# Performance work log

Measured on AMD Instinct MI355X. Metric: run time of the kernel, lower is better.

Reference implementation:

```python
import jax, jax.numpy as jnp
import numpy as np

B, S, DIN, DIM = 4, 4096, 256, 256
GAMMA = 0.9865


def setup_inputs() -> dict:
    key = jax.random.key(0)
    ks = jax.random.split(key, 9)
    inp = {
        'xq': jax.random.normal(ks[0], (B, S, DIN), dtype=jnp.float32),
        'xk': jax.random.normal(ks[1], (B, S, DIN), dtype=jnp.float32),
        'xv': jax.random.normal(ks[2], (B, S, DIN), dtype=jnp.float32),
        'Wq': jax.random.normal(ks[3], (DIN, DIM), dtype=jnp.float32) * 0.05,
        'bq': jnp.zeros((DIM,), dtype=jnp.float32),
        'Wk': jax.random.normal(ks[4], (DIN, DIM), dtype=jnp.float32) * 0.05,
        'bk': jnp.zeros((DIM,), dtype=jnp.float32),
        'Wv': jax.random.normal(ks[5], (DIN, DIM), dtype=jnp.float32) * 0.05,
        'bv': jnp.zeros((DIM,), dtype=jnp.float32),
    }
    return inp


def _decay_matrix(s, gamma):
    # D[i, j] = gamma^(i-j) if i >= j else 0
    idx = jnp.arange(s)
    diff = idx[:, None] - idx[None, :]
    D = jnp.where(diff >= 0,
                  jnp.power(jnp.float32(gamma), diff.astype(jnp.float32)),
                  jnp.float32(0.0))
    return D


def reference(xq, xk, xv, Wq, bq, Wk, bk, Wv, bv):
    Q = xq @ Wq + bq  # [B,S,D]
    K = xk @ Wk + bk  # [B,S,D]
    V = xv @ Wv + bv  # [B,S,D]
    d = Q.shape[-1]
    # scores[b,i,j] = Q[b,i] . K[b,j] / sqrt(d)
    x = jnp.einsum('bid,bjd->bij', Q, K) / jnp.sqrt(jnp.float32(d))
    D = _decay_matrix(S, GAMMA)
    # Faithful to TF broadcasting: divides along the LAST axis (per-column by
    # sqrt of that index's row-sum): D[i,j] /= sqrt(sum_k D[j,k])
    D = D / jnp.sqrt(jnp.sum(D, axis=-1))
    x = x * D  # broadcast [B,S,S] * [S,S]
    # _norm_3 per batch element with TF broadcasting: x[b,i,j] /= max(|sum_k x[b,j,k]|, 1)
    denom = jnp.maximum(jnp.abs(jnp.sum(x, axis=-1)), 1.0)  # [B,S]
    x = x / denom[:, None, :]
    return x @ V  # [B,S,D]
```

## Files before the change

### kernel.cpp

```cpp
#include <hip/hip_runtime.h>
#include <math.h>

#define BB 4
#define SS 4096
#define DD 256
#define LL 256
#define NCH 16
#define GAMMA 0.9865f
#define LOG2G (-0.019609034f)
#define INV1MG 74.07407407f
#define SLAB 1032
#define SLABB 520

typedef __attribute__((ext_vector_type(8))) short short8;
typedef __attribute__((ext_vector_type(4))) float f32x4;
typedef unsigned short u16;
typedef unsigned int u32;

__device__ __forceinline__ u16 f2bf(float f) {
  union { float f; unsigned u; } v; v.f = f;
  unsigned r = v.u + 0x7FFFu + ((v.u >> 16) & 1u);
  return (u16)(r >> 16);
}
__device__ __forceinline__ float bf2f(u16 h) {
  union { unsigned u; float f; } v; v.u = ((unsigned)h) << 16; return v.f;
}

__device__ __forceinline__ void gll16(const u16* g, u16* l) {
  __builtin_amdgcn_global_load_lds(
      (const __attribute__((address_space(1))) u32*)g,
      (__attribute__((address_space(3))) u32*)l, 16, 0, 0);
}
__device__ __forceinline__ void stage8kp(const u16* g, u16* l, int lane) {
#pragma unroll
  for (int i = 0; i < 8; ++i)
    gll16(g + i * 512 + lane * 8, l + (i >> 1) * SLAB + (i & 1) * 512);
}
__device__ __forceinline__ void stageB64(const u16* g, u16* l, int lane) {
#pragma unroll
  for (int i = 0; i < 4; ++i)
    gll16(g + i * 1024 + lane * 8, l + i * SLABB);
}
__device__ __forceinline__ void stageAB(
    const u16* AhP, const u16* AlP, const u16* BhP, const u16* BlP, int ks,
    u16* Ab, u16* Bb, int wave, int lane)
{
  if (wave == 0) stage8kp(AhP + ks * 4096, Ab, lane);
  if (wave == 1) stage8kp(AlP + ks * 4096, Ab + 4 * SLAB, lane);
  if (wave == 2) stageB64(BhP + ks * 4096, Bb, lane);
  if (wave == 3) stageB64(BlP + ks * 4096, Bb + 4 * SLABB, lane);
}

__device__ __forceinline__ void mfma_step_slab(
    const u16* Ah, const u16* Al, const u16* Bh, const u16* Bl,
    int wm0, int wn0, int fm, int fq, f32x4 acc[4][4])
{
  const int ka = fq * SLAB;
  short8 ah[4], al[4];
#pragma unroll
  for (int i = 0; i < 4; ++i) {
    ah[i] = *(const short8*)&Ah[ka + (wm0 + i * 16 + fm) * 8];
    al[i] = *(const short8*)&Al[ka + (wm0 + i * 16 + fm) * 8];
  }
#pragma unroll
  for (int j = 0; j < 4; ++j) {
    short8 bh = *(const short8*)&Bh[ka + (wn0 + j * 16 + fm) * 8];
    short8 bl = *(const short8*)&Bl[ka + (wn0 + j * 16 + fm) * 8];
#pragma unroll
    for (int i = 0; i < 4; ++i) {
      acc[i][j] = __builtin_amdgcn_mfma_f32_16x16x32_bf16(al[i], bh, acc[i][j], 0, 0, 0);
      acc[i][j] = __builtin_amdgcn_mfma_f32_16x16x32_bf16(ah[i], bl, acc[i][j], 0, 0, 0);
      acc[i][j] = __builtin_amdgcn_mfma_f32_16x16x32_bf16(ah[i], bh, acc[i][j], 0, 0, 0);
    }
  }
}

__device__ __forceinline__ void mfma_step_ab(
    const u16* Ah, const u16* Al, const u16* Bh, const u16* Bl,
    int wm0, int wn0, int fm, int fq, f32x4 acc[4][2])
{
  const int ka = fq * SLAB, kb = fq * SLABB;
  short8 ah[4], al[4];
#pragma unroll
  for (int i = 0; i < 4; ++i) {
    ah[i] = *(const short8*)&Ah[ka + (wm0 + i * 16 + fm) * 8];
    al[i] = *(const short8*)&Al[ka + (wm0 + i * 16 + fm) * 8];
  }
#pragma unroll
  for (int j = 0; j < 2; ++j) {
    short8 bh = *(const short8*)&Bh[kb + (wn0 + j * 16 + fm) * 8];
    short8 bl = *(const short8*)&Bl[kb + (wn0 + j * 16 + fm) * 8];
#pragma unroll
    for (int i = 0; i < 4; ++i) {
      acc[i][j] = __builtin_amdgcn_mfma_f32_16x16x32_bf16(al[i], bh, acc[i][j], 0, 0, 0);
      acc[i][j] = __builtin_amdgcn_mfma_f32_16x16x32_bf16(ah[i], bl, acc[i][j], 0, 0, 0);
      acc[i][j] = __builtin_amdgcn_mfma_f32_16x16x32_bf16(ah[i], bh, acc[i][j], 0, 0, 0);
    }
  }
}

__device__ __forceinline__ void bounce_write(
    float* fb, const f32x4 acc[4][4], int wm0, int wn0, int fm, int fq, int p)
{
  if (wn0 == p * 64) {
#pragma unroll
    for (int i = 0; i < 4; ++i)
#pragma unroll
      for (int j = 0; j < 4; ++j)
#pragma unroll
        for (int r = 0; r < 4; ++r)
          fb[(wm0 + i * 16 + fq * 4 + r) * 65 + j * 16 + fm] = acc[i][j][r];
  }
}

__global__ __launch_bounds__(256) void init_pack_kernel(
    const float* __restrict__ Wq, const float* __restrict__ Wk, const float* __restrict__ Wv,
    u16* __restrict__ Wth, u16* __restrict__ Wtl,
    float* __restrict__ rsP, float* __restrict__ lVec)
{
  const int which = blockIdx.x;
  const int it = blockIdx.y;
  const int t = threadIdx.x;
  if (which == 0) {
    *(float4*)&rsP[(size_t)(it * 256 + t) * 4] = (float4){0.f, 0.f, 0.f, 0.f};
  } else if (which == 1) {
    *(float4*)&lVec[(size_t)(it * 256 + t) * 4] = (float4){0.f, 0.f, 0.f, 0.f};
  }
  const float* W = which == 0 ? Wq : (which == 1 ? Wk : Wv);
  for (int pn = 0; pn < 2; ++pn) {
    int pos = it * 256 + t;
    int k8 = pos >> 7, r = pos & 127;
    u16 hs[8], ls[8];
#pragma unroll
    for (int u = 0; u < 8; ++u) {
      float x = W[(size_t)(k8 * 8 + u) * DD + pn * 128 + r];
      u16 h = f2bf(x); hs[u] = h; ls[u] = f2bf(x - bf2f(h));
    }
    size_t o = ((size_t)((which * 2 + pn) * 32 + k8)) * 1024 + (size_t)r * 8;
    *(short8*)&Wth[o] = *(short8*)hs;
    *(short8*)&Wtl[o] = *(short8*)ls;
  }
}

__device__ __forceinline__ void loadX(float xs[2][8], const float* XP, int ks,
                                      int arow, int ak8) {
#pragma unroll
  for (int t = 0; t < 2; ++t) {
    const float* src = XP + (size_t)(t * 64 + arow) * DD + ks * 32 + ak8 * 8;
    *(float4*)&xs[t][0] = *(const float4*)src;
    *(float4*)&xs[t][4] = *(const float4*)(src + 4);
  }
}
__device__ __forceinline__ void writeAsplit(u16* Ab, const float xs[2][8],
                                            int arow, int ak8) {
#pragma unroll
  for (int t = 0; t < 2; ++t) {
    int row = t * 64 + arow;
    u16 hs[8], ls[8];
#pragma unroll
    for (int u = 0; u < 8; ++u) {
      u16 h = f2bf(xs[t][u]); hs[u] = h; ls[u] = f2bf(xs[t][u] - bf2f(h));
    }
    *(short8*)&Ab[ak8 * SLAB + row * 8] = *(short8*)hs;
    *(short8*)&Ab[4 * SLAB + ak8 * SLAB + row * 8] = *(short8*)ls;
  }
}

__global__ __launch_bounds__(256, 2) void proj_kernel(
    const float* __restrict__ xq, const float* __restrict__ xk, const float* __restrict__ xv,
    const u16* __restrict__ Wth, const u16* __restrict__ Wtl,
    const float* __restrict__ bq, const float* __restrict__ bk_, const float* __restrict__ bv,
    u16* __restrict__ Qh, u16* __restrict__ Ql,
    u16* __restrict__ Kh, u16* __restrict__ Kl,
    u16* __restrict__ KTh, u16* __restrict__ KTl, float* __restrict__ VT32,
    float* __restrict__ lVec)
{
  const int which = blockIdx.z;
  const float* bias = which == 0 ? bq : (which == 1 ? bk_ : bv);
  const int m0 = blockIdx.x * 128;
  const int pn = blockIdx.y;
  __shared__ u16 SM[2 * 16 * SLAB];
  __shared__ float rsc[128];
  __shared__ float wlut[128];
  __shared__ float kacc[64];
  float* fb = (float*)SM;
  const int tid = threadIdx.x, lane = tid & 63, wave = tid >> 6;
  const int wm0 = (wave >> 1) * 64, wn0 = (wave & 1) * 64;
  const int fm = lane & 15, fq = lane >> 4;
  if (which == 1) {
    if (tid < 128) {
      int sb = (m0 & (SS - 1)) + tid;
      rsc[tid] = rsqrtf((1.0f - exp2f((float)(sb + 1) * LOG2G)) * INV1MG);
      wlut[tid] = exp2f((float)(255 - ((m0 & (LL - 1)) + tid)) * LOG2G);
    }
    if (tid < 64) kacc[tid] = 0.f;
  }
  const float* XP = (which == 0 ? xq : (which == 1 ? xk : xv)) + (size_t)m0 * DD;
  const u16* WhP = Wth + (size_t)((which * 2 + pn) * 32) * 1024;
  const u16* WlP = Wtl + (size_t)((which * 2 + pn) * 32) * 1024;
  const int arow = tid >> 2, ak8 = tid & 3;
  f32x4 acc[4][4];
#pragma unroll
  for (int i = 0; i < 4; ++i)
#pragma unroll
    for (int j = 0; j < 4; ++j) acc[i][j] = (f32x4){0.f, 0.f, 0.f, 0.f};
  float xs[2][8];
  loadX(xs, XP, 0, arow, ak8);
  writeAsplit(SM, xs, arow, ak8);
  if (wave == 2) stage8kp(WhP, SM + 8 * SLAB, lane);
  if (wave == 3) stage8kp(WlP, SM + 12 * SLAB, lane);
  int cur = 0;
  for (int ks = 0; ks < 8; ++ks) {
    __syncthreads();
    u16* Bc = cur ? SM + 16 * SLAB : SM;
    u16* Bn = cur ? SM : SM + 16 * SLAB;
    if (ks < 7) {
      loadX(xs, XP, ks + 1, arow, ak8);
      if (wave == 2) stage8kp(WhP + (ks + 1) * 4096, Bn + 8 * SLAB, lane);
      if (wave == 3) stage8kp(WlP + (ks + 1) * 4096, Bn + 12 * SLAB, lane);
    }
    mfma_step_slab(Bc, Bc + 4 * SLAB, Bc + 8 * SLAB, Bc + 12 * SLAB,
                   wm0, wn0, fm, fq, acc);
    if (ks < 7) writeAsplit(Bn, xs, arow, ak8);
    cur ^= 1;
  }
  const int b = m0 >> 12, sbb = m0 & (SS - 1);
  for (int p = 0; p < 2; ++p) {
    __syncthreads();
    bounce_write(fb, acc, wm0, wn0, fm, fq, p);
    __syncthreads();
    if (which == 0) {
#pragma unroll
      for (int it = 0; it < 4; ++it) {
        int unit = it * 256 + tid;
        int k8l = unit >> 7, row = unit & 127;
        int gcol0 = pn * 128 + p * 64 + k8l * 8;
        u16 hs[8], ls[8];
#pragma unroll
        for (int u = 0; u < 8; ++u) {
          float v = (fb[row * 65 + k8l * 8 + u] + bias[gcol0 + u]) * (1.f / 16.f);
          u16 h = f2bf(v); hs[u] = h; ls[u] = f2bf(v - bf2f(h));
        }
        size_t o = (size_t)(m0 >> 7) * 32768 + (size_t)(pn * 16 + p * 8 + k8l) * 1024 + row * 8;
        *(short8*)&Qh[o] = *(short8*)hs;
        *(short8*)&Ql[o] = *(short8*)ls;
      }
    } else if (which == 1) {
#pragma unroll
      for (int it = 0; it < 4; ++it) {
        int unit = it * 256 + tid;
        int k8l = unit >> 7, row = unit & 127;
        int gcol0 = pn * 128 + p * 64 + k8l * 8;
        u16 hs[8], ls[8];
#pragma unroll
        for (int u = 0; u < 8; ++u) {
          float v = (fb[row * 65 + k8l * 8 + u] + bias[gcol0 + u]) * rsc[row];
          u16 h = f2bf(v); hs[u] = h; ls[u] = f2bf(v - bf2f(h));
        }
        size_t o = (size_t)(m0 >> 7) * 32768 + (size_t)(pn * 16 + p * 8 + k8l) * 1024 + row * 8;
        *(short8*)&Kh[o] = *(short8*)hs;
        *(short8*)&Kl[o] = *(short8*)ls;
      }
      float kpart = 0.f;
#pragma unroll
      for (int it = 0; it < 4; ++it) {
        int unit = it * 256 + tid;
        int dl = unit & 63, s8l = unit >> 6;
        int gcolg = pn * 128 + p * 64 + dl;
        float bs = bias[gcolg];
        u16 hs[8], ls[8];
#pragma unroll
        for (int u = 0; u < 8; ++u) {
          int row = s8l * 8 + u;
          float v = (fb[row * 65 + dl] + bs) * rsc[row];
          kpart = fmaf(v, wlut[row], kpart);
          u16 h = f2bf(v); hs[u] = h; ls[u] = f2bf(v - bf2f(h));
        }
        int sb0 = sbb + s8l * 8;
        size_t o = ((size_t)(b * 2 + (gcolg >> 7)) * 512 + (sb0 >> 3)) * 1024 + (size_t)(gcolg & 127) * 8;
        *(short8*)&KTh[o] = *(short8*)hs;
        *(short8*)&KTl[o] = *(short8*)ls;
      }
      atomicAdd(&kacc[tid & 63], kpart);
      __syncthreads();
      if (tid < 64) {
        int c = sbb >> 8;
        atomicAdd(&lVec[(size_t)(b * NCH + c) * DD + pn * 128 + p * 64 + tid], kacc[tid]);
        kacc[tid] = 0.f;
      }
    } else {
#pragma unroll
      for (int it = 0; it < 4; ++it) {
        int unit = it * 256 + tid;
        int dl = unit & 63, s8l = unit >> 6;
        int gcolg = pn * 128 + p * 64 + dl;
        float bs = bias[gcolg];
        float vv[8];
#pragma unroll
        for (int u = 0; u < 8; ++u) vv[u] = fb[(s8l * 8 + u) * 65 + dl] + bs;
        float* dst = &VT32[(size_t)b * DD * SS + (size_t)gcolg * SS + sbb + s8l * 8];
        *(float4*)dst = (float4){vv[0], vv[1], vv[2], vv[3]};
        *(float4*)(dst + 4) = (float4){vv[4], vv[5], vv[6], vv[7]};
      }
    }
  }
}

__global__ __launch_bounds__(256, 3) void scores_kernel(
    const u16* __restrict__ Qh, const u16* __restrict__ Ql,
    const u16* __restrict__ Kh, const u16* __restrict__ Kl,
    const float* __restrict__ lVec, u16* __restrict__ Sgh, u16* __restrict__ Sgl,
    float* __restrict__ rsP)
{
  const int chunk = blockIdx.x, b = chunk >> 4, c = chunk & 15;
  const int y = blockIdx.y;
  const int m0 = (y < 2) ? 0 : 128;
  const int jn0 = (y < 2) ? y * 64 : (y - 2) * 64;
  __shared__ u16 SA[2 * 8 * SLAB];
  __shared__ u16 SB[2 * 8 * SLABB];
  __shared__ float cv[256], lut[256], rowAcc[128], qd2[2][128];
  float* fb = (float*)SA;
  const int tid = threadIdx.x, lane = tid & 63, wave = tid >> 6;
  const int wm0 = (wave >> 1) * 64, wn0 = (wave & 1) * 32;
  const int fm = lane & 15, fq = lane >> 4;
  if (jn0 == 0) {
    const float gL = exp2f((float)LL * LOG2G);
    float s = 0.f;
    for (int cp = 0; cp < c; ++cp)
      s = fmaf(gL, s, lVec[(size_t)(b * NCH + cp) * DD + tid]);
    cv[tid] = s;
  }
  lut[tid] = exp2f((float)tid * LOG2G);
  if (tid < 128) rowAcc[tid] = 0.f;
  const int growA = b * SS + c * LL + m0;
  const int growB = b * SS + c * LL + jn0;
  const u16* QhP = Qh + (size_t)(growA >> 7) * 32768;
  const u16* QlP = Ql + (size_t)(growA >> 7) * 32768;
  const u16* KhP = Kh + (size_t)(growB >> 7) * 32768 + (size_t)(growB & 127) * 8;
  const u16* KlP = Kl + (size_t)(growB >> 7) * 32768 + (size_t)(growB & 127) * 8;
  f32x4 acc[4][2];
#pragma unroll
  for (int i = 0; i < 4; ++i)
#pragma unroll
    for (int j = 0; j < 2; ++j) acc[i][j] = (f32x4){0.f, 0.f, 0.f, 0.f};
  float qdreg = 0.f;
  const int qrow = tid & 127, qk8b = tid >> 7;
  stageAB(QhP, QlP, KhP, KlP, 0, SA, SB, wave, lane);
  int cur = 0;
  for (int ks = 0; ks < 8; ++ks) {
    __syncthreads();
    u16* Ac = cur ? SA + 8 * SLAB : SA;
    u16* Bc = cur ? SB + 8 * SLABB : SB;
    u16* An = cur ? SA : SA + 8 * SLAB;
    u16* Bn = cur ? SB : SB + 8 * SLABB;
    if (ks < 7) stageAB(QhP, QlP, KhP, KlP, ks + 1, An, Bn, wave, lane);
    mfma_step_ab(Ac, Ac + 4 * SLAB, Bc, Bc + 4 * SLABB, wm0, wn0, fm, fq, acc);
    if (jn0 == 0) {
#pragma unroll
      for (int h2 = 0; h2 < 2; ++h2) {
        int k8l = qk8b + 2 * h2;
        const u16* ahp = &Ac[k8l * SLAB + qrow * 8];
        const u16* alp = &Ac[4 * SLAB + k8l * SLAB + qrow * 8];
#pragma unroll
        for (int u = 0; u < 8; ++u)
          qdreg = fmaf(bf2f(ahp[u]) + bf2f(alp[u]), cv[ks * 32 + k8l * 8 + u], qdreg);
      }
    }
    cur ^= 1;
  }
  qd2[qk8b][qrow] = qdreg;
  const int ps = chunk * 2 + (m0 >> 7);
  for (int rh = 0; rh < 2; ++rh) {
    __syncthreads();
    if (wm0 == rh * 64) {
#pragma unroll
      for (int i = 0; i < 4; ++i)
#pragma unroll
        for (int j = 0; j < 2; ++j)
#pragma unroll
          for (int r = 0; r < 4; ++r)
            fb[(i * 16 + fq * 4 + r) * 65 + wn0 + j * 16 + fm] = acc[i][j][r];
    }
    __syncthreads();
#pragma unroll
    for (int it = 0; it < 2; ++it) {
      int unit = it * 256 + tid;
      int k8l = unit >> 6, rowl = unit & 63;
      int il = m0 + rh * 64 + rowl;
      int jlb = jn0 + k8l * 8;
      float part = 0.f;
      u16 hs[8], ls[8];
#pragma unroll
      for (int u = 0; u < 8; ++u) {
        int jl = jlb + u;
        float v = (jl <= il) ? fb[rowl * 65 + k8l * 8 + u] * lut[il - jl] : 0.f;
        part += v;
        u16 h = f2bf(v); hs[u] = h; ls[u] = f2bf(v - bf2f(h));
      }
      atomicAdd(&rowAcc[rh * 64 + rowl], part);
      size_t o = (size_t)(ps * 32 + (jn0 >> 3) + k8l) * 1024 + (size_t)(rh * 64 + rowl) * 8;
      *(short8*)&Sgh[o] = *(short8*)hs;
      *(short8*)&Sgl[o] = *(short8*)ls;
    }
  }
  __syncthreads();
  if (tid < 128) {
    float rs = rowAcc[tid];
    if (jn0 == 0)
      rs += exp2f((float)(m0 + tid + 1) * LOG2G) * (qd2[0][tid] + qd2[1][tid]);
    atomicAdd(&rsP[(size_t)b * SS + c * LL + m0 + tid], rs);
  }
}

__global__ __launch_bounds__(256) void vscale_kernel(
    const float* __restrict__ VT32, const float* __restrict__ rsP,
    u16* __restrict__ VdTh, u16* __restrict__ VdTl,
    u16* __restrict__ VwTh, u16* __restrict__ VwTl)
{
  const int x = blockIdx.x;
  const int b = x >> 6, pd = (x >> 5) & 1, sg = x & 31;
  const int t = threadIdx.x;
  __shared__ float tile[64][132];
  __shared__ float sdn[128], wtl[128];
  if (t < 128) {
    int s = sg * 128 + t;
    sdn[t] = fmaxf(fabsf(rsP[(size_t)b * SS + s]), 1.0f);
    wtl[t] = exp2f((float)(255 - (s & 255)) * LOG2G);
  }
  for (int eh = 0; eh < 2; ++eh) {
    __syncthreads();
#pragma unroll
    for (int v = 0; v < 8; ++v) {
      int lin = v * 256 + t;
      int col4 = lin & 31, row = lin >> 5;
      float4 xv = *(const float4*)&VT32[(size_t)b * DD * SS +
          (size_t)(pd * 128 + eh * 64 + row) * SS + sg * 128 + col4 * 4];
      *(float4*)&tile[row][col4 * 4] = xv;
    }
    __syncthreads();
#pragma unroll
    for (int it = 0; it < 4; ++it) {
      int unit = it * 256 + t;
      int s8l = unit >> 6, el = unit & 63;
      int e = pd * 128 + eh * 64 + el;
      u16 dh[8], dl_[8], wh[8], wl[8];
#pragma unroll
      for (int u = 0; u < 8; ++u) {
        int sloc = s8l * 8 + u;
        float vd = tile[el][sloc] / sdn[sloc];
        float vw = vd * wtl[sloc];
        u16 h = f2bf(vd); dh[u] = h; dl_[u] = f2bf(vd - bf2f(h));
        u16 h2 = f2bf(vw); wh[u] = h2; wl[u] = f2bf(vw - bf2f(h2));
      }
      int s8g = sg * 16 + s8l;
      size_t o = ((size_t)((b * 2 + pd) * 512 + s8g)) * 1024 + (size_t)(e & 127) * 8;
      *(short8*)&VdTh[o] = *(short8*)dh; *(short8*)&VdTl[o] = *(short8*)dl_;
      *(short8*)&VwTh[o] = *(short8*)wh; *(short8*)&VwTl[o] = *(short8*)wl;
    }
  }
}

__global__ __launch_bounds__(256, 3) void lmat_kernel(
    const u16* __restrict__ VwTh, const u16* __restrict__ VwTl,
    const u16* __restrict__ KTh, const u16* __restrict__ KTl,
    float* __restrict__ lMatT)
{
  const int chunk = blockIdx.x, b = chunk >> 4, c = chunk & 15;
  const int ty = blockIdx.y;
  const int m0 = (ty >> 2) * 128, n0 = (ty & 3) * 64;
  __shared__ u16 SA[2 * 8 * SLAB];
  __shared__ u16 SB[2 * 8 * SLABB];
  const int tid = threadIdx.x, lane = tid & 63, wave = tid >> 6;
  const int wm0 = (wave >> 1) * 64, wn0 = (wave & 1) * 32;
  const int fm = lane & 15, fq = lane >> 4;
  const u16* AhP = VwTh + ((size_t)(b * 2 + (m0 >> 7)) * 512 + c * 32) * 1024;
  const u16* AlP = VwTl + ((size_t)(b * 2 + (m0 >> 7)) * 512 + c * 32) * 1024;
  const u16* BhP = KTh + ((size_t)(b * 2 + (n0 >> 7)) * 512 + c * 32) * 1024 + (size_t)(n0 & 127) * 8;
  const u16* BlP = KTl + ((size_t)(b * 2 + (n0 >> 7)) * 512 + c * 32) * 1024 + (size_t)(n0 & 127) * 8;
  f32x4 acc[4][2];
#pragma unroll
  for (int i = 0; i < 4; ++i)
#pragma unroll
    for (int j = 0; j < 2; ++j) acc[i][j] = (f32x4){0.f, 0.f, 0.f, 0.f};
  stageAB(AhP, AlP, BhP, BlP, 0, SA, SB, wave, lane);
  int cur = 0;
  for (int ks = 0; ks < 8; ++ks) {
    __syncthreads();
    u16* Ac = cur ? SA + 8 * SLAB : SA;
    u16* Bc = cur ? SB + 8 * SLABB : SB;
    u16* An = cur ? SA : SA + 8 * SLAB;
    u16* Bn = cur ? SB : SB + 8 * SLABB;
    if (ks < 7) stageAB(AhP, AlP, BhP, BlP, ks + 1, An, Bn, wave, lane);
    mfma_step_ab(Ac, Ac + 4 * SLAB, Bc, Bc + 4 * SLABB, wm0, wn0, fm, fq, acc);
    cur ^= 1;
  }
#pragma unroll
  for (int i = 0; i < 4; ++i)
#pragma unroll
    for (int j = 0; j < 2; ++j)
#pragma unroll
      for (int r = 0; r < 4; ++r) {
        int e = m0 + wm0 + i * 16 + fq * 4 + r;
        int d = n0 + wn0 + j * 16 + fm;
        lMatT[(size_t)chunk * 65536 + (size_t)e * 256 + d] = acc[i][j][r];
      }
}

__global__ __launch_bounds__(256) void combine_mat_kernel(
    const float* __restrict__ lMatT, u16* __restrict__ cMh, u16* __restrict__ cMl)
{
  const int t = blockIdx.x * 256 + threadIdx.x;
  const int b = t >> 13, rem = t & 8191;
  const int k8 = rem >> 8, e = rem & 255;
  const float gL = powf(GAMMA, (float)LL);
  float s[8] = {0.f, 0.f, 0.f, 0.f, 0.f, 0.f, 0.f, 0.f};
  for (int ch = 0; ch < 16; ++ch) {
    size_t ro = (size_t)(b * 16 + ch) * 65536 + (size_t)e * 256 + k8 * 8;
    float4 a0 = *(const float4*)&lMatT[ro];
    float4 a1 = *(const float4*)&lMatT[ro + 4];
    float vals[8] = {a0.x, a0.y, a0.z, a0.w, a1.x, a1.y, a1.z, a1.w};
    u16 hh[8], ll[8];
#pragma unroll
    for (int u = 0; u < 8; ++u) {
      u16 h = f2bf(s[u]); hh[u] = h; ll[u] = f2bf(s[u] - bf2f(h));
    }
    size_t wo = ((size_t)(((b * 16 + ch) * 2 + (e >> 7)) * 32 + k8)) * 1024 + (size_t)(e & 127) * 8;
    *(short8*)&cMh[wo] = *(short8*)hh;
    *(short8*)&cMl[wo] = *(short8*)ll;
#pragma unroll
    for (int u = 0; u < 8; ++u) s[u] = gL * s[u] + vals[u];
  }
}

__global__ __launch_bounds__(256, 3) void out_kernel(
    const u16* __restrict__ Qh, const u16* __restrict__ Ql,
    const u16* __restrict__ cMh, const u16* __restrict__ cMl,
    const u16* __restrict__ Sgh, const u16* __restrict__ Sgl,
    const u16* __restrict__ VdTh, const u16* __restrict__ VdTl,
    float* __restrict__ out)
{
  const int chunk = blockIdx.x, b = chunk >> 4, c = chunk & 15;
  const int ty = blockIdx.y;
  const int m0 = (ty >> 2) * 128, n0 = (ty & 3) * 64;
  __shared__ u16 SA[2 * 8 * SLAB];
  __shared__ u16 SB[2 * 8 * SLABB];
  __shared__ float olut[128];
  const int tid = threadIdx.x, lane = tid & 63, wave = tid >> 6;
  const int wm0 = (wave >> 1) * 64, wn0 = (wave & 1) * 32;
  const int fm = lane & 15, fq = lane >> 4;
  if (tid < 128) olut[tid] = exp2f((float)(m0 + tid + 1) * LOG2G);
  f32x4 acc[4][2];
#pragma unroll
  for (int i = 0; i < 4; ++i)
#pragma unroll
    for (int j = 0; j < 2; ++j) acc[i][j] = (f32x4){0.f, 0.f, 0.f, 0.f};
  int cur = 0;
  {
    const u16* AhP = Qh + (size_t)(b * 32 + c * 2 + (m0 >> 7)) * 32768;
    const u16* AlP = Ql + (size_t)(b * 32 + c * 2 + (m0 >> 7)) * 32768;
    const u16* BhP = cMh + (size_t)(chunk * 2 + (n0 >> 7)) * 32768 + (size_t)(n0 & 127) * 8;
    const u16* BlP = cMl + (size_t)(chunk * 2 + (n0 >> 7)) * 32768 + (size_t)(n0 & 127) * 8;
    stageAB(AhP, AlP, BhP, BlP, 0, SA, SB, wave, lane);
    for (int ks = 0; ks < 8; ++ks) {
      __syncthreads();
      u16* Ac = cur ? SA + 8 * SLAB : SA;
      u16* Bc = cur ? SB + 8 * SLABB : SB;
      u16* An = cur ? SA : SA + 8 * SLAB;
      u16* Bn = cur ? SB : SB + 8 * SLABB;
      if (ks < 7) stageAB(AhP, AlP, BhP, BlP, ks + 1, An, Bn, wave, lane);
      mfma_step_ab(Ac, Ac + 4 * SLAB, Bc, Bc + 4 * SLABB, wm0, wn0, fm, fq, acc);
      cur ^= 1;
    }
  }
  {
    const u16* AhP = Sgh + (size_t)(chunk * 2 + (m0 >> 7)) * 32768;
    const u16* AlP = Sgl + (size_t)(chunk * 2 + (m0 >> 7)) * 32768;
    const u16* BhP = VdTh + ((size_t)(b * 2 + (n0 >> 7)) * 512 + c * 32) * 1024 + (size_t)(n0 & 127) * 8;
    const u16* BlP = VdTl + ((size_t)(b * 2 + (n0 >> 7)) * 512 + c * 32) * 1024 + (size_t)(n0 & 127) * 8;
    const int nks = (m0 >> 5) + 4;
    {
      u16* Ac = cur ? SA + 8 * SLAB : SA;
      u16* Bc = cur ? SB + 8 * SLABB : SB;
      stageAB(AhP, AlP, BhP, BlP, 0, Ac, Bc, wave, lane);
    }
#pragma unroll
    for (int i = 0; i < 4; ++i)
#pragma unroll
      for (int r = 0; r < 4; ++r) {
        int rl = wm0 + i * 16 + fq * 4 + r;
        float sc = olut[rl];
#pragma unroll
        for (int j = 0; j < 2; ++j) acc[i][j][r] *= sc;
      }
    for (int ks = 0; ks < nks; ++ks) {
      __syncthreads();
      u16* Ac = cur ? SA + 8 * SLAB : SA;
      u16* Bc = cur ? SB + 8 * SLABB : SB;
      u16* An = cur ? SA : SA + 8 * SLAB;
      u16* Bn = cur ? SB : SB + 8 * SLABB;
      if (ks + 1 < nks) stageAB(AhP, AlP, BhP, BlP, ks + 1, An, Bn, wave, lane);
      mfma_step_ab(Ac, Ac + 4 * SLAB, Bc, Bc + 4 * SLABB, wm0, wn0, fm, fq, acc);
      cur ^= 1;
    }
  }
#pragma unroll
  for (int i = 0; i < 4; ++i)
#pragma unroll
    for (int j = 0; j < 2; ++j)
#pragma unroll
      for (int r = 0; r < 4; ++r) {
        int il = m0 + wm0 + i * 16 + fq * 4 + r;
        int e = n0 + wn0 + j * 16 + fm;
        out[(size_t)(b * SS + c * LL + il) * DD + e] = acc[i][j][r];
      }
}

extern "C" void kernel_launch(void* const* d_in, const int* in_sizes, int n_in,
                              void* d_out, int out_size, void* d_ws, size_t ws_size,
                              hipStream_t stream) {
  const float* xq = (const float*)d_in[0];
  const float* xk = (const float*)d_in[1];
  const float* xv = (const float*)d_in[2];
  const float* Wq = (const float*)d_in[3];
  const float* bq = (const float*)d_in[4];
  const float* Wk = (const float*)d_in[5];
  const float* bk = (const float*)d_in[6];
  const float* Wv = (const float*)d_in[7];
  const float* bv = (const float*)d_in[8];
  float* out = (float*)d_out;

  char* p = (char*)d_ws;
  const size_t H16 = (size_t)BB * SS * DD * 2;
  u16* Qh   = (u16*)(p + 0 * H16);  u16* Ql   = (u16*)(p + 1 * H16);
  u16* Kh   = (u16*)(p + 2 * H16);  u16* Kl   = (u16*)(p + 3 * H16);
  u16* KTh  = (u16*)(p + 4 * H16);  u16* KTl  = (u16*)(p + 5 * H16);
  u16* VdTh = (u16*)(p + 6 * H16);  u16* VdTl = (u16*)(p + 7 * H16);
  u16* VwTh = (u16*)(p + 8 * H16);  u16* VwTl = (u16*)(p + 9 * H16);
  u16* Sgh  = (u16*)(p + 10 * H16); u16* Sgl  = (u16*)(p + 11 * H16);
  u16* cMh  = (u16*)(p + 12 * H16); u16* cMl  = (u16*)(p + 13 * H16);
  float* lMatT = (float*)(p + 14 * H16);
  float* VT32  = (float*)(p + 16 * H16);
  u16* Wth = (u16*)(p + 18 * H16);
  u16* Wtl = (u16*)(p + 18 * H16 + 3 * DD * DD * 2);
  float* rsP  = (float*)(p + 18 * H16 + 6 * DD * DD * 2);
  float* lVec = rsP + (size_t)BB * SS;

  init_pack_kernel<<<dim3(3, 16), 256, 0, stream>>>(Wq, Wk, Wv, Wth, Wtl, rsP, lVec);
  proj_kernel<<<dim3(BB * SS / 128, 2, 3), 256, 0, stream>>>(
      xq, xk, xv, Wth, Wtl, bq, bk, bv, Qh, Ql, Kh, Kl, KTh, KTl, VT32, lVec);
  scores_kernel<<<dim3(BB * NCH, 6), 256, 0, stream>>>(
      Qh, Ql, Kh, Kl, lVec, Sgh, Sgl, rsP);
  vscale_kernel<<<256, 256, 0, stream>>>(VT32, rsP, VdTh, VdTl, VwTh, VwTl);
  lmat_kernel<<<dim3(BB * NCH, 8), 256, 0, stream>>>(VwTh, VwTl, KTh, KTl, lMatT);
  combine_mat_kernel<<<128, 256, 0, stream>>>(lMatT, cMh, cMl);
  out_kernel<<<dim3(BB * NCH, 8), 256, 0, stream>>>(
      Qh, Ql, cMh, cMl, Sgh, Sgl, VdTh, VdTl, out);
}
```

Measured before the change: 211.5 us.

## Fuse V scaling and bf16 split into lmat and out kernel staging

```diff
diff --git a/kernel.cpp b/kernel.cpp
--- a/kernel.cpp
+++ b/kernel.cpp
@@ -412,56 +412,8 @@
   }
 }
 
-__global__ __launch_bounds__(256) void vscale_kernel(
+__global__ __launch_bounds__(256, 3) void lmat_kernel(
     const float* __restrict__ VT32, const float* __restrict__ rsP,
-    u16* __restrict__ VdTh, u16* __restrict__ VdTl,
-    u16* __restrict__ VwTh, u16* __restrict__ VwTl)
-{
-  const int x = blockIdx.x;
-  const int b = x >> 6, pd = (x >> 5) & 1, sg = x & 31;
-  const int t = threadIdx.x;
-  __shared__ float tile[64][132];
-  __shared__ float sdn[128], wtl[128];
-  if (t < 128) {
-    int s = sg * 128 + t;
-    sdn[t] = fmaxf(fabsf(rsP[(size_t)b * SS + s]), 1.0f);
-    wtl[t] = exp2f((float)(255 - (s & 255)) * LOG2G);
-  }
-  for (int eh = 0; eh < 2; ++eh) {
-    __syncthreads();
-#pragma unroll
-    for (int v = 0; v < 8; ++v) {
-      int lin = v * 256 + t;
-      int col4 = lin & 31, row = lin >> 5;
-      float4 xv = *(const float4*)&VT32[(size_t)b * DD * SS +
-          (size_t)(pd * 128 + eh * 64 + row) * SS + sg * 128 + col4 * 4];
-      *(float4*)&tile[row][col4 * 4] = xv;
-    }
-    __syncthreads();
-#pragma unroll
-    for (int it = 0; it < 4; ++it) {
-      int unit = it * 256 + t;
-      int s8l = unit >> 6, el = unit & 63;
-      int e = pd * 128 + eh * 64 + el;
-      u16 dh[8], dl_[8], wh[8], wl[8];
-#pragma unroll
-      for (int u = 0; u < 8; ++u) {
-        int sloc = s8l * 8 + u;
-        float vd = tile[el][sloc] / sdn[sloc];
-        float vw = vd * wtl[sloc];
-        u16 h = f2bf(vd); dh[u] = h; dl_[u] = f2bf(vd - bf2f(h));
-        u16 h2 = f2bf(vw); wh[u] = h2; wl[u] = f2bf(vw - bf2f(h2));
-      }
-      int s8g = sg * 16 + s8l;
-      size_t o = ((size_t)((b * 2 + pd) * 512 + s8g)) * 1024 + (size_t)(e & 127) * 8;
-      *(short8*)&VdTh[o] = *(short8*)dh; *(short8*)&VdTl[o] = *(short8*)dl_;
-      *(short8*)&VwTh[o] = *(short8*)wh; *(short8*)&VwTl[o] = *(short8*)wl;
-    }
-  }
-}
-
-__global__ __launch_bounds__(256, 3) void lmat_kernel(
-    const u16* __restrict__ VwTh, const u16* __restrict__ VwTl,
     const u16* __restrict__ KTh, const u16* __restrict__ KTl,
     float* __restrict__ lMatT)
 {
@@ -470,19 +422,44 @@
   const int m0 = (ty >> 2) * 128, n0 = (ty & 3) * 64;
   __shared__ u16 SA[2 * 8 * SLAB];
   __shared__ u16 SB[2 * 8 * SLABB];
+  __shared__ float swl[256];
   const int tid = threadIdx.x, lane = tid & 63, wave = tid >> 6;
   const int wm0 = (wave >> 1) * 64, wn0 = (wave & 1) * 32;
   const int fm = lane & 15, fq = lane >> 4;
-  const u16* AhP = VwTh + ((size_t)(b * 2 + (m0 >> 7)) * 512 + c * 32) * 1024;
-  const u16* AlP = VwTl + ((size_t)(b * 2 + (m0 >> 7)) * 512 + c * 32) * 1024;
+  swl[tid] = exp2f((float)(255 - tid) * LOG2G) /
+             fmaxf(fabsf(rsP[(size_t)b * SS + c * LL + tid]), 1.0f);
+  const float* AP = VT32 + (size_t)b * DD * SS + (size_t)m0 * SS + c * LL;
   const u16* BhP = KTh + ((size_t)(b * 2 + (n0 >> 7)) * 512 + c * 32) * 1024 + (size_t)(n0 & 127) * 8;
   const u16* BlP = KTl + ((size_t)(b * 2 + (n0 >> 7)) * 512 + c * 32) * 1024 + (size_t)(n0 & 127) * 8;
+  const int arow = tid >> 1;
   f32x4 acc[4][2];
 #pragma unroll
   for (int i = 0; i < 4; ++i)
 #pragma unroll
     for (int j = 0; j < 2; ++j) acc[i][j] = (f32x4){0.f, 0.f, 0.f, 0.f};
-  stageAB(AhP, AlP, BhP, BlP, 0, SA, SB, wave, lane);
+  float as[2][8];
+#pragma unroll
+  for (int t = 0; t < 2; ++t) {
+    int ak8 = (tid & 1) * 2 + t;
+    const float* src = AP + (size_t)arow * SS + ak8 * 8;
+    *(float4*)&as[t][0] = *(const float4*)src;
+    *(float4*)&as[t][4] = *(const float4*)(src + 4);
+  }
+  __syncthreads();
+#pragma unroll
+  for (int t = 0; t < 2; ++t) {
+    int ak8 = (tid & 1) * 2 + t;
+    u16 hs[8], ls[8];
+#pragma unroll
+    for (int u = 0; u < 8; ++u) {
+      float v = as[t][u] * swl[ak8 * 8 + u];
+      u16 h = f2bf(v); hs[u] = h; ls[u] = f2bf(v - bf2f(h));
+    }
+    *(short8*)&SA[ak8 * SLAB + arow * 8] = *(short8*)hs;
+    *(short8*)&SA[4 * SLAB + ak8 * SLAB + arow * 8] = *(short8*)ls;
+  }
+  if (wave == 2) stageB64(BhP, SB, lane);
+  if (wave == 3) stageB64(BlP, SB + 4 * SLABB, lane);
   int cur = 0;
   for (int ks = 0; ks < 8; ++ks) {
     __syncthreads();
@@ -490,8 +467,32 @@
     u16* Bc = cur ? SB + 8 * SLABB : SB;
     u16* An = cur ? SA : SA + 8 * SLAB;
     u16* Bn = cur ? SB : SB + 8 * SLABB;
-    if (ks < 7) stageAB(AhP, AlP, BhP, BlP, ks + 1, An, Bn, wave, lane);
+    if (ks < 7) {
+#pragma unroll
+      for (int t = 0; t < 2; ++t) {
+        int ak8 = (tid & 1) * 2 + t;
+        const float* src = AP + (size_t)arow * SS + (ks + 1) * 32 + ak8 * 8;
+        *(float4*)&as[t][0] = *(const float4*)src;
+        *(float4*)&as[t][4] = *(const float4*)(src + 4);
+      }
+      if (wave == 2) stageB64(BhP + (ks + 1) * 4096, Bn, lane);
+      if (wave == 3) stageB64(BlP + (ks + 1) * 4096, Bn + 4 * SLABB, lane);
+    }
     mfma_step_ab(Ac, Ac + 4 * SLAB, Bc, Bc + 4 * SLABB, wm0, wn0, fm, fq, acc);
+    if (ks < 7) {
+#pragma unroll
+      for (int t = 0; t < 2; ++t) {
+        int ak8 = (tid & 1) * 2 + t;
+        u16 hs[8], ls[8];
+#pragma unroll
+        for (int u = 0; u < 8; ++u) {
+          float v = as[t][u] * swl[(ks + 1) * 32 + ak8 * 8 + u];
+          u16 h = f2bf(v); hs[u] = h; ls[u] = f2bf(v - bf2f(h));
+        }
+        *(short8*)&An[ak8 * SLAB + arow * 8] = *(short8*)hs;
+        *(short8*)&An[4 * SLAB + ak8 * SLAB + arow * 8] = *(short8*)ls;
+      }
+    }
     cur ^= 1;
   }
 #pragma unroll
@@ -536,7 +537,7 @@
     const u16* __restrict__ Qh, const u16* __restrict__ Ql,
     const u16* __restrict__ cMh, const u16* __restrict__ cMl,
     const u16* __restrict__ Sgh, const u16* __restrict__ Sgl,
-    const u16* __restrict__ VdTh, const u16* __restrict__ VdTl,
+    const float* __restrict__ VT32, const float* __restrict__ rsP,
     float* __restrict__ out)
 {
   const int chunk = blockIdx.x, b = chunk >> 4, c = chunk & 15;
@@ -545,10 +546,12 @@
   __shared__ u16 SA[2 * 8 * SLAB];
   __shared__ u16 SB[2 * 8 * SLABB];
   __shared__ float olut[128];
+  __shared__ float sdn[256];
   const int tid = threadIdx.x, lane = tid & 63, wave = tid >> 6;
   const int wm0 = (wave >> 1) * 64, wn0 = (wave & 1) * 32;
   const int fm = lane & 15, fq = lane >> 4;
   if (tid < 128) olut[tid] = exp2f((float)(m0 + tid + 1) * LOG2G);
+  sdn[tid] = 1.0f / fmaxf(fabsf(rsP[(size_t)b * SS + c * LL + tid]), 1.0f);
   f32x4 acc[4][2];
 #pragma unroll
   for (int i = 0; i < 4; ++i)
@@ -575,31 +578,60 @@
   {
     const u16* AhP = Sgh + (size_t)(chunk * 2 + (m0 >> 7)) * 32768;
     const u16* AlP = Sgl + (size_t)(chunk * 2 + (m0 >> 7)) * 32768;
-    const u16* BhP = VdTh + ((size_t)(b * 2 + (n0 >> 7)) * 512 + c * 32) * 1024 + (size_t)(n0 & 127) * 8;
-    const u16* BlP = VdTl + ((size_t)(b * 2 + (n0 >> 7)) * 512 + c * 32) * 1024 + (size_t)(n0 & 127) * 8;
+    const float* BP = VT32 + (size_t)b * DD * SS + (size_t)n0 * SS + c * LL;
+    const int ber = tid >> 2, bk8 = tid & 3;
     const int nks = (m0 >> 5) + 4;
+    float bs[8];
     {
       u16* Ac = cur ? SA + 8 * SLAB : SA;
       u16* Bc = cur ? SB + 8 * SLABB : SB;
-      stageAB(AhP, AlP, BhP, BlP, 0, Ac, Bc, wave, lane);
-    }
-#pragma unroll
-    for (int i = 0; i < 4; ++i)
-#pragma unroll
-      for (int r = 0; r < 4; ++r) {
-        int rl = wm0 + i * 16 + fq * 4 + r;
-        float sc = olut[rl];
-#pragma unroll
-        for (int j = 0; j < 2; ++j) acc[i][j][r] *= sc;
-      }
+      if (wave == 0) stage8kp(AhP, Ac, lane);
+      if (wave == 1) stage8kp(AlP, Ac + 4 * SLAB, lane);
+      const float* src = BP + (size_t)ber * SS + bk8 * 8;
+      *(float4*)&bs[0] = *(const float4*)src;
+      *(float4*)&bs[4] = *(const float4*)(src + 4);
+#pragma unroll
+      for (int i = 0; i < 4; ++i)
+#pragma unroll
+        for (int r = 0; r < 4; ++r) {
+          int rl = wm0 + i * 16 + fq * 4 + r;
+          float sc = olut[rl];
+#pragma unroll
+          for (int j = 0; j < 2; ++j) acc[i][j][r] *= sc;
+        }
+      u16 hs[8], ls[8];
+#pragma unroll
+      for (int u = 0; u < 8; ++u) {
+        float v = bs[u] * sdn[bk8 * 8 + u];
+        u16 h = f2bf(v); hs[u] = h; ls[u] = f2bf(v - bf2f(h));
+      }
+      *(short8*)&Bc[bk8 * SLABB + ber * 8] = *(short8*)hs;
+      *(short8*)&Bc[4 * SLABB + bk8 * SLABB + ber * 8] = *(short8*)ls;
+    }
     for (int ks = 0; ks < nks; ++ks) {
       __syncthreads();
       u16* Ac = cur ? SA + 8 * SLAB : SA;
       u16* Bc = cur ? SB + 8 * SLABB : SB;
       u16* An = cur ? SA : SA + 8 * SLAB;
       u16* Bn = cur ? SB : SB + 8 * SLABB;
-      if (ks + 1 < nks) stageAB(AhP, AlP, BhP, BlP, ks + 1, An, Bn, wave, lane);
+      if (ks + 1 < nks) {
+        if (wave == 0) stage8kp(AhP + (ks + 1) * 4096, An, lane);
+        if (wave == 1) stage8kp(AlP + (ks + 1) * 4096, An + 4 * SLAB, lane);
+        const float* src = BP + (size_t)ber * SS + (ks + 1) * 32 + bk8 * 8;
+        *(float4*)&bs[0] = *(const float4*)src;
+        *(float4*)&bs[4] = *(const float4*)(src + 4);
+      }
       mfma_step_ab(Ac, Ac + 4 * SLAB, Bc, Bc + 4 * SLABB, wm0, wn0, fm, fq, acc);
+      if (ks + 1 < nks) {
+        u16 hs[8], ls[8];
+#pragma unroll
+        for (int u = 0; u < 8; ++u) {
+          float v = bs[u] * sdn[(ks + 1) * 32 + bk8 * 8 + u];
+          u16 h = f2bf(v); hs[u] = h; ls[u] = f2bf(v - bf2f(h));
+        }
+        *(short8*)&Bn[bk8 * SLABB + ber * 8] = *(short8*)hs;
+        *(short8*)&Bn[4 * SLABB + bk8 * SLABB + ber * 8] = *(short8*)ls;
+      }
       cur ^= 1;
     }
   }
@@ -634,8 +666,6 @@
   u16* Qh   = (u16*)(p + 0 * H16);  u16* Ql   = (u16*)(p + 1 * H16);
   u16* Kh   = (u16*)(p + 2 * H16);  u16* Kl   = (u16*)(p + 3 * H16);
   u16* KTh  = (u16*)(p + 4 * H16);  u16* KTl  = (u16*)(p + 5 * H16);
-  u16* VdTh = (u16*)(p + 6 * H16);  u16* VdTl = (u16*)(p + 7 * H16);
-  u16* VwTh = (u16*)(p + 8 * H16);  u16* VwTl = (u16*)(p + 9 * H16);
   u16* Sgh  = (u16*)(p + 10 * H16); u16* Sgl  = (u16*)(p + 11 * H16);
   u16* cMh  = (u16*)(p + 12 * H16); u16* cMl  = (u16*)(p + 13 * H16);
   float* lMatT = (float*)(p + 14 * H16);
@@ -650,9 +680,8 @@
       xq, xk, xv, Wth, Wtl, bq, bk, bv, Qh, Ql, Kh, Kl, KTh, KTl, VT32, lVec);
   scores_kernel<<<dim3(BB * NCH, 6), 256, 0, stream>>>(
       Qh, Ql, Kh, Kl, lVec, Sgh, Sgl, rsP);
-  vscale_kernel<<<256, 256, 0, stream>>>(VT32, rsP, VdTh, VdTl, VwTh, VwTl);
-  lmat_kernel<<<dim3(BB * NCH, 8), 256, 0, stream>>>(VwTh, VwTl, KTh, KTl, lMatT);
+  lmat_kernel<<<dim3(BB * NCH, 8), 256, 0, stream>>>(VT32, rsP, KTh, KTl, lMatT);
   combine_mat_kernel<<<128, 256, 0, stream>>>(lMatT, cMh, cMl);
   out_kernel<<<dim3(BB * NCH, 8), 256, 0, stream>>>(
-      Qh, Ql, cMh, cMl, Sgh, Sgl, VdTh, VdTl, out);
-}
+      Qh, Ql, cMh, cMl, Sgh, Sgl, VT32, rsP, out);
+}
```

Measured after the change: 206.2 us. 1.03x faster.
